# Optimization experiments

Hardware: AMD Instinct MI355X
Metric: run time of the kernel (lower is better)

The kernel has to match this reference:

```python
import jax, jax.numpy as jnp
import numpy as np

N_NODES = 20000
N_EDGES = 640000
NODE_DIM = 128
HIDDEN_DIM = 256
OUTPUT_DIM = 128


def setup_inputs() -> dict:
    key = jax.random.key(0)
    ks = jax.random.split(key, 10)
    x = jax.random.normal(ks[0], (N_NODES, NODE_DIM), dtype=jnp.float32)
    edge_index = jax.random.randint(ks[1], (2, N_EDGES), 0, N_NODES, dtype=jnp.int64)
    s1 = 1.0 / np.sqrt(2 * NODE_DIM)
    s1b = 1.0 / np.sqrt(HIDDEN_DIM)
    s2 = 1.0 / np.sqrt(2 * HIDDEN_DIM)
    s2b = 1.0 / np.sqrt(OUTPUT_DIM)
    # layer 1 MLP: Linear(2*node_dim, hidden) -> ReLU -> Linear(hidden, hidden)
    W1a = jax.random.uniform(ks[2], (2 * NODE_DIM, HIDDEN_DIM), jnp.float32, -s1, s1)
    b1a = jax.random.uniform(ks[3], (HIDDEN_DIM,), jnp.float32, -s1, s1)
    W1b = jax.random.uniform(ks[4], (HIDDEN_DIM, HIDDEN_DIM), jnp.float32, -s1b, s1b)
    b1b = jax.random.uniform(ks[5], (HIDDEN_DIM,), jnp.float32, -s1b, s1b)
    # layer 2 MLP: Linear(2*hidden, output) -> ReLU -> Linear(output, output)
    W2a = jax.random.uniform(ks[6], (2 * HIDDEN_DIM, OUTPUT_DIM), jnp.float32, -s2, s2)
    b2a = jax.random.uniform(ks[7], (OUTPUT_DIM,), jnp.float32, -s2, s2)
    W2b = jax.random.uniform(ks[8], (OUTPUT_DIM, OUTPUT_DIM), jnp.float32, -s2b, s2b)
    b2b = jax.random.uniform(ks[9], (OUTPUT_DIM,), jnp.float32, -s2b, s2b)
    return {"x": x, "edge_index": edge_index,
            "W1a": W1a, "b1a": b1a, "W1b": W1b, "b1b": b1b,
            "W2a": W2a, "b2a": b2a, "W2b": W2b, "b2b": b2b}


def _gnn_layer(x, src, dst, Wa, ba, Wb, bb):
    # PyG source_to_target: x_j = x[src], x_i = x[dst]; message on cat([x_i, x_j])
    h = jnp.concatenate([x[dst], x[src]], axis=-1)          # [E, 2D]
    m = jax.nn.relu(h @ Wa + ba) @ Wb + bb                  # [E, Dout]
    agg = jax.ops.segment_sum(m, dst, num_segments=N_NODES)  # [N, Dout]
    cnt = jax.ops.segment_sum(jnp.ones((m.shape[0],), m.dtype), dst,
                              num_segments=N_NODES)
    return agg / jnp.maximum(cnt, 1.0)[:, None]             # scatter-mean (0 if no edges)


def reference(x, edge_index, W1a, b1a, W1b, b1b, W2a, b2a, W2b, b2b):
    src = edge_index[0]
    dst = edge_index[1]
    h = jax.nn.relu(_gnn_layer(x, src, dst, W1a, b1a, W1b, b1b))
    out = _gnn_layer(h, src, dst, W2a, b2a, W2b, b2b)
    return out
```

## Files before the change

### kernel.cpp

```cpp
#include <hip/hip_runtime.h>


#define NODE_DIM 128
#define HID 256
#define OUTD 128
#define CPAD 16
#define SLOTS 128

typedef __attribute__((ext_vector_type(8))) _Float16 f16x8;
typedef __attribute__((ext_vector_type(4))) float f32x4;
typedef __attribute__((ext_vector_type(2))) _Float16 h2;

__device__ __forceinline__ h2 bc2(unsigned u) {
    return __builtin_bit_cast(h2, u);
}
__device__ __forceinline__ ushort f2h(float x) {
    _Float16 h = (_Float16)x;
    return __builtin_bit_cast(ushort, h);
}

__global__ void prep_all(const float* __restrict__ W1a, const float* __restrict__ W1b,
                         const float* __restrict__ W2a, const float* __restrict__ W2b,
                         ushort* __restrict__ T1a, ushort* __restrict__ T1b,
                         ushort* __restrict__ T2a, ushort* __restrict__ T2b,
                         int* __restrict__ cnt_p, int N) {
    int j = blockIdx.x * blockDim.x + threadIdx.x;
    if (j < 65536) {
        int n = j >> 7, k = j & 127;
        float v = (n < 256) ? W1a[k * 256 + n] : W1a[(128 + k) * 256 + (n - 256)];
        T1a[j] = f2h(v);
        return;
    }
    if (j < 131072) {
        int t = j - 65536;
        int n = t >> 8, k = t & 255;
        T1b[t] = f2h(W1b[k * 256 + n]);
        return;
    }
    if (j < 196608) {
        int t = j - 131072;
        int n = t >> 8, k = t & 255;
        float v = (n < 128) ? W2a[k * 128 + n] : W2a[(256 + k) * 128 + (n - 128)];
        T2a[t] = f2h(v);
        return;
    }
    if (j < 212992) {
        int t = j - 196608;
        int n = t >> 7, k = t & 127;
        T2b[t] = f2h(W2b[k * 128 + n]);
        return;
    }
    int k = j - 212992;
    if (k < N * CPAD) cnt_p[k] = 0;
}

__global__ void scatter_hist(const int* __restrict__ src, const int* __restrict__ dst,
                             int* __restrict__ cnt_p, int* __restrict__ csr, int E) {
    int e = (blockIdx.x * blockDim.x + threadIdx.x) * 2;
    if (e + 1 < E) {
        int2 s = *(const int2*)(src + e);
        int2 d = *(const int2*)(dst + e);
        int p0 = atomicAdd(&cnt_p[(size_t)d.x * CPAD], 1);
        if (p0 < SLOTS) csr[(size_t)d.x * SLOTS + p0] = s.x;
        int p1 = atomicAdd(&cnt_p[(size_t)d.y * CPAD], 1);
        if (p1 < SLOTS) csr[(size_t)d.y * SLOTS + p1] = s.y;
    } else if (e < E) {
        int p = atomicAdd(&cnt_p[(size_t)dst[e] * CPAD], 1);
        if (p < SLOTS) csr[(size_t)dst[e] * SLOTS + p] = src[e];
    }
}


#define GBM 128
#define GBN 128
#define GBK 32
#define LDSW 40

template <int MODE, int AF32>
__global__ __launch_bounds__(256) void gemm_h(
    const void* __restrict__ Av, int M, int K,
    const ushort* __restrict__ BT,
    const float* __restrict__ bias, const int* __restrict__ gate, int gstride,
    int relu, float* __restrict__ Cf, ushort* __restrict__ Ch, int Nc, int nsplit) {
    __shared__ ushort sA[GBM * LDSW];
    __shared__ ushort sB[GBN * LDSW];

    const int tid = threadIdx.x;
    const int lane = tid & 63;
    const int w = tid >> 6;
    const int wm = w >> 1, wn = w & 1;
    const int r16 = lane & 15, kg = lane >> 4;
    const int m0 = blockIdx.x * GBM;
    const int n0 = blockIdx.y * GBN;

    const int arow = tid >> 1, ahalf = tid & 1;

    f32x4 acc[4][4];
#pragma unroll
    for (int i = 0; i < 4; i++)
#pragma unroll
        for (int j = 0; j < 4; j++) acc[i][j] = (f32x4)0.f;

    for (int kt = 0; kt < K; kt += GBK) {
        {
            const int gr = m0 + arow;
            ushort* d = sA + arow * LDSW + ahalf * 16;
            if constexpr (AF32) {
                const float* Af = (const float*)Av;
                float4 v0 = make_float4(0.f, 0.f, 0.f, 0.f), v1 = v0, v2 = v0, v3 = v0;
                if (gr < M) {
                    const float* p = Af + (size_t)gr * K + kt + ahalf * 16;
                    v0 = ((const float4*)p)[0];
                    v1 = ((const float4*)p)[1];
                    v2 = ((const float4*)p)[2];
                    v3 = ((const float4*)p)[3];
                }
                ushort4 h0, h1, h2_, h3;
                h0.x = f2h(v0.x); h0.y = f2h(v0.y); h0.z = f2h(v0.z); h0.w = f2h(v0.w);
                h1.x = f2h(v1.x); h1.y = f2h(v1.y); h1.z = f2h(v1.z); h1.w = f2h(v1.w);
                h2_.x = f2h(v2.x); h2_.y = f2h(v2.y); h2_.z = f2h(v2.z); h2_.w = f2h(v2.w);
                h3.x = f2h(v3.x); h3.y = f2h(v3.y); h3.z = f2h(v3.z); h3.w = f2h(v3.w);
                ((ushort4*)d)[0] = h0;
                ((ushort4*)d)[1] = h1;
                ((ushort4*)d)[2] = h2_;
                ((ushort4*)d)[3] = h3;
            } else {
                const ushort* Ah = (const ushort*)Av;
                const size_t go = (size_t)gr * K + kt + ahalf * 16;
                int4 a0 = make_int4(0, 0, 0, 0), a1 = a0;
                if (gr < M) {
                    a0 = *(const int4*)(Ah + go);
                    a1 = *(const int4*)(Ah + go + 8);
                }
                *(int4*)(d) = a0;
                *(int4*)(d + 8) = a1;
            }
        }
        {
            const size_t go = (size_t)(n0 + arow) * K + kt + ahalf * 16;
            int4 b0 = *(const int4*)(BT + go);
            int4 b1 = *(const int4*)(BT + go + 8);
            ushort* d = sB + arow * LDSW + ahalf * 16;
            *(int4*)(d) = b0;
            *(int4*)(d + 8) = b1;
        }
        __syncthreads();

        f16x8 av[4], bv[4];
#pragma unroll
        for (int mi = 0; mi < 4; mi++)
            av[mi] = *(const f16x8*)(sA + (wm * 64 + mi * 16 + r16) * LDSW + kg * 8);
#pragma unroll
        for (int ni = 0; ni < 4; ni++)
            bv[ni] = *(const f16x8*)(sB + (wn * 64 + ni * 16 + r16) * LDSW + kg * 8);
#pragma unroll
        for (int mi = 0; mi < 4; mi++)
#pragma unroll
            for (int ni = 0; ni < 4; ni++)
                acc[mi][ni] = __builtin_amdgcn_mfma_f32_16x16x32_f16(av[mi], bv[ni], acc[mi][ni], 0, 0, 0);
        __syncthreads();
    }

#pragma unroll
    for (int ni = 0; ni < 4; ni++) {
        const int col = n0 + wn * 64 + ni * 16 + r16;
        float bv = 0.f;
        if constexpr (MODE == 1) {
            bv = (col < nsplit && bias) ? bias[col] : 0.f;
        } else {
            bv = bias ? bias[col] : 0.f;
        }
#pragma unroll
        for (int mi = 0; mi < 4; mi++) {
#pragma unroll
            for (int r = 0; r < 4; r++) {
                const int row = m0 + wm * 64 + mi * 16 + kg * 4 + r;
                if (row >= M) continue;
                if constexpr (MODE == 1) {
                    const float v = acc[mi][ni][r];
                    if (col < nsplit) {
                        Cf[(size_t)row * nsplit + col] = v + bv;
                    } else {
                        Ch[(size_t)row * (Nc - nsplit) + (col - nsplit)] = f2h(v);
                    }
                } else {
                    float g = 1.f;
                    if (gate) g = (gate[(size_t)row * gstride] > 0) ? 1.f : 0.f;
                    float v = acc[mi][ni][r] + bv * g;
                    if (relu) v = fmaxf(v, 0.f);
                    const size_t o = (size_t)row * Nc + col;
                    if constexpr (MODE == 0) {
                        Cf[o] = v;
                    } else {
                        Ch[o] = f2h(v);
                    }
                }
            }
        }
    }
}


template <int H>
__global__ __launch_bounds__(256) void agg_f(const float* __restrict__ Ptop,
                                             const ushort* __restrict__ Pbot,
                                             const int* __restrict__ cnt_p,
                                             const int* __restrict__ csr,
                                             ushort* __restrict__ S, int N) {
    constexpr int VPL = H / 64;
    __shared__ float red[2][64 * VPL];

    const int tid = threadIdx.x;
    const int lane = tid & 63;
    const int wv = __builtin_amdgcn_readfirstlane(tid >> 6);
    const int nb = wv >> 1;
    const int sub = wv & 1;
    int n = blockIdx.x * 2 + nb;
    if (n >= N) n = N - 1;

    int deg = cnt_p[(size_t)n * CPAD];
    if (deg > SLOTS) deg = SLOTS;
    const int begin = n * SLOTS;

    h2 t01, t23;
    if constexpr (VPL == 4) {
        float4 tf = *(const float4*)(Ptop + (size_t)n * H + lane * 4);
        t01 = (h2){(_Float16)tf.x, (_Float16)tf.y};
        t23 = (h2){(_Float16)tf.z, (_Float16)tf.w};
    } else {
        float2 tf = *(const float2*)(Ptop + (size_t)n * H + lane * 2);
        t01 = (h2){(_Float16)tf.x, (_Float16)tf.y};
        t23 = t01;
    }
    const h2 z2 = (h2)(_Float16)0.f;

    float a0 = 0.f, a1 = 0.f, a2 = 0.f, a3 = 0.f;
    const ushort* pb = Pbot + lane * VPL;

    const int Gf = deg >> 3;
    const int r = deg & 7;

    for (int g = sub; g < Gf; g += 2) {
        const int e = begin + g * 8;
        h2 p01 = z2, p23 = z2;
#pragma unroll
        for (int j = 0; j < 8; j++) {
            const int idx = csr[e + j];
            if constexpr (VPL == 4) {
                uint2 u = *(const uint2*)(pb + (size_t)idx * H);
                p01 += __builtin_elementwise_max(t01 + bc2(u.x), z2);
                p23 += __builtin_elementwise_max(t23 + bc2(u.y), z2);
            } else {
                unsigned u = *(const unsigned*)(pb + (size_t)idx * H);
                p01 += __builtin_elementwise_max(t01 + bc2(u), z2);
            }
        }
        a0 += (float)p01.x;
        a1 += (float)p01.y;
        if constexpr (VPL == 4) {
            a2 += (float)p23.x;
            a3 += (float)p23.y;
        }
    }
    if (r && sub == (Gf & 1)) {
        const int e = begin + Gf * 8;
        h2 p01 = z2, p23 = z2;
        for (int j = 0; j < r; j++) {
            const int idx = csr[e + j];
            if constexpr (VPL == 4) {
                uint2 u = *(const uint2*)(pb + (size_t)idx * H);
                p01 += __builtin_elementwise_max(t01 + bc2(u.x), z2);
                p23 += __builtin_elementwise_max(t23 + bc2(u.y), z2);
            } else {
                unsigned u = *(const unsigned*)(pb + (size_t)idx * H);
                p01 += __builtin_elementwise_max(t01 + bc2(u), z2);
            }
        }
        a0 += (float)p01.x;
        a1 += (float)p01.y;
        if constexpr (VPL == 4) {
            a2 += (float)p23.x;
            a3 += (float)p23.y;
        }
    }

    if (sub == 1) {
        red[nb][lane * VPL + 0] = a0;
        red[nb][lane * VPL + 1] = a1;
        if constexpr (VPL == 4) {
            red[nb][lane * VPL + 2] = a2;
            red[nb][lane * VPL + 3] = a3;
        }
    }
    __syncthreads();
    if (sub == 0) {
        a0 += red[nb][lane * VPL + 0];
        a1 += red[nb][lane * VPL + 1];
        if constexpr (VPL == 4) {
            a2 += red[nb][lane * VPL + 2];
            a3 += red[nb][lane * VPL + 3];
        }
        const float inv = (deg > 0) ? 1.f / (float)deg : 0.f;
        if constexpr (VPL == 4) {
            ushort4 h;
            h.x = f2h(a0 * inv);
            h.y = f2h(a1 * inv);
            h.z = f2h(a2 * inv);
            h.w = f2h(a3 * inv);
            *(ushort4*)(S + (size_t)n * H + lane * 4) = h;
        } else {
            ushort2 h;
            h.x = f2h(a0 * inv);
            h.y = f2h(a1 * inv);
            *(ushort2*)(S + (size_t)n * H + lane * 2) = h;
        }
    }
}


extern "C" void kernel_launch(void* const* d_in, const int* in_sizes, int n_in,
                              void* d_out, int out_size, void* d_ws, size_t ws_size,
                              hipStream_t stream) {
    const int N = in_sizes[0] / NODE_DIM;
    const int E = in_sizes[1] / 2;

    const float* x = (const float*)d_in[0];
    const int* ei = (const int*)d_in[1];
    const int* e_src = ei;
    const int* e_dst = ei + E;
    const float* W1a = (const float*)d_in[2];
    const float* b1a = (const float*)d_in[3];
    const float* W1b = (const float*)d_in[4];
    const float* b1b = (const float*)d_in[5];
    const float* W2a = (const float*)d_in[6];
    const float* b2a = (const float*)d_in[7];
    const float* W2b = (const float*)d_in[8];
    const float* b2b = (const float*)d_in[9];

    char* ws = (char*)d_ws;
    size_t off = 0;
    auto alloc = [&](size_t bytes) {
        size_t o = off;
        off += (bytes + 255) & ~(size_t)255;
        return o;
    };
    int* cnt_p = (int*)(ws + alloc((size_t)N * CPAD * 4));
    int* csr = (int*)(ws + alloc((size_t)N * SLOTS * 4));
    ushort* T1a = (ushort*)(ws + alloc((size_t)(2 * HID) * NODE_DIM * 2));
    ushort* T1b = (ushort*)(ws + alloc((size_t)HID * HID * 2));
    ushort* T2a = (ushort*)(ws + alloc((size_t)(2 * OUTD) * HID * 2));
    ushort* T2b = (ushort*)(ws + alloc((size_t)OUTD * OUTD * 2));
    float* P1t = (float*)(ws + alloc((size_t)N * HID * 4));
    ushort* P1b = (ushort*)(ws + alloc((size_t)N * HID * 2));
    ushort* P2b = (ushort*)(ws + alloc((size_t)N * OUTD * 2));
    ushort* S1 = (ushort*)(ws + alloc((size_t)N * HID * 2));
    ushort* S2 = (ushort*)(ws + alloc((size_t)N * OUTD * 2));
    ushort* h_h = (ushort*)(ws + alloc((size_t)N * HID * 2));
    float* P2t = P1t;

    const int MT = (N + GBM - 1) / GBM;
    const int AG = (N + 1) / 2;

    const int prep_n = 212992 + N * CPAD;
    prep_all<<<(prep_n + 255) / 256, 256, 0, stream>>>(
        W1a, W1b, W2a, W2b, T1a, T1b, T2a, T2b, cnt_p, N);

    scatter_hist<<<((E + 1) / 2 + 255) / 256, 256, 0, stream>>>(e_src, e_dst, cnt_p, csr, E);

    gemm_h<1, 1><<<dim3(MT, (2 * HID) / GBN), 256, 0, stream>>>(
        x, N, NODE_DIM, T1a, b1a, nullptr, 0, 0, P1t, P1b, 2 * HID, HID);

    agg_f<HID><<<AG, 256, 0, stream>>>(P1t, P1b, cnt_p, csr, S1, N);

    gemm_h<3, 0><<<dim3(MT, HID / GBN), 256, 0, stream>>>(
        S1, N, HID, T1b, b1b, cnt_p, CPAD, 1, nullptr, h_h, HID, 0);

    gemm_h<1, 0><<<dim3(MT, (2 * OUTD) / GBN), 256, 0, stream>>>(
        h_h, N, HID, T2a, b2a, nullptr, 0, 0, P2t, P2b, 2 * OUTD, OUTD);

    agg_f<OUTD><<<AG, 256, 0, stream>>>(P2t, P2b, cnt_p, csr, S2, N);

    gemm_h<0, 0><<<dim3(MT, OUTD / GBN), 256, 0, stream>>>(
        S2, N, OUTD, T2b, b2b, cnt_p, CPAD, 0, (float*)d_out, nullptr, OUTD, 0);
}
```

Before: 182.6 us.

## Slice aggregation by feature quarter per XCD with sentinel-padded neighbor lists

The aggregation kernel is rewritten so that each wave handles one node over a 64-feature slice. Blocks are mapped so that each XCD always works on the same feature slice, which keeps the gathered rows of that slice hot in its local L2. Neighbor lists are padded to multiples of 32 with a sentinel node index that points at an extra row filled with -inf half values, so the padded terms contribute zero after ReLU. This removes the remainder loop and the cross-wave LDS reduction and batches eight gathers before use. In exchange it adds a full csr initialization pass in the prep kernel, does up to 31 wasted gathers per node, and relies on blockIdx-to-XCD round-robin placement.

```diff
diff --git a/kernel.cpp b/kernel.cpp
--- a/kernel.cpp
+++ b/kernel.cpp
@@ -23,7 +23,9 @@
                          const float* __restrict__ W2a, const float* __restrict__ W2b,
                          ushort* __restrict__ T1a, ushort* __restrict__ T1b,
                          ushort* __restrict__ T2a, ushort* __restrict__ T2b,
-                         int* __restrict__ cnt_p, int N) {
+                         int* __restrict__ cnt_p, int N,
+                         ushort* __restrict__ P1b, ushort* __restrict__ P2b,
+                         int* __restrict__ csr) {
     int j = blockIdx.x * blockDim.x + threadIdx.x;
     if (j < 65536) {
         int n = j >> 7, k = j & 127;
@@ -51,7 +53,24 @@
         return;
     }
     int k = j - 212992;
-    if (k < N * CPAD) cnt_p[k] = 0;
+    if (k < N * CPAD) {
+        cnt_p[k] = 0;
+        return;
+    }
+    k -= N * CPAD;
+    if (k < HID) {
+        P1b[(size_t)N * HID + k] = 0xFC00;
+        return;
+    }
+    k -= HID;
+    if (k < OUTD) {
+        P2b[(size_t)N * OUTD + k] = 0xFC00;
+        return;
+    }
+    k -= OUTD;
+    if (k < N * SLOTS / 4) {
+        ((int4*)csr)[k] = make_int4(N, N, N, N);
+    }
 }
 
 __global__ void scatter_hist(const int* __restrict__ src, const int* __restrict__ dst,
@@ -202,118 +221,79 @@
 
 
 template <int H>
-__global__ __launch_bounds__(256) void agg_f(const float* __restrict__ Ptop,
+__global__ __launch_bounds__(256) void agg_s(const float* __restrict__ Ptop,
                                              const ushort* __restrict__ Pbot,
                                              const int* __restrict__ cnt_p,
                                              const int* __restrict__ csr,
                                              ushort* __restrict__ S, int N) {
-    constexpr int VPL = H / 64;
-    __shared__ float red[2][64 * VPL];
-
-    const int tid = threadIdx.x;
-    const int lane = tid & 63;
-    const int wv = __builtin_amdgcn_readfirstlane(tid >> 6);
-    const int nb = wv >> 1;
-    const int sub = wv & 1;
-    int n = blockIdx.x * 2 + nb;
-    if (n >= N) n = N - 1;
+    constexpr int SLICES = H / 64;
+    constexpr int XPS = 8 / SLICES;
+
+    const int bid = blockIdx.x;
+    const int xcd = bid & 7;
+    const int grp = bid >> 3;
+    const int slice = xcd / XPS;
+    const int subx = xcd % XPS;
+    const int wave = threadIdx.x >> 6;
+    const int lane = threadIdx.x & 63;
+
+    const int n = (grp * XPS + subx) * 4 + wave;
+    if (n >= N) return;
+    const int qoff = slice * 64;
+
+    const int fq = lane & 15;
+    const int es = lane >> 4;
 
     int deg = cnt_p[(size_t)n * CPAD];
     if (deg > SLOTS) deg = SLOTS;
+    const int dpad = (deg + 31) & ~31;
     const int begin = n * SLOTS;
 
-    h2 t01, t23;
-    if constexpr (VPL == 4) {
-        float4 tf = *(const float4*)(Ptop + (size_t)n * H + lane * 4);
-        t01 = (h2){(_Float16)tf.x, (_Float16)tf.y};
-        t23 = (h2){(_Float16)tf.z, (_Float16)tf.w};
-    } else {
-        float2 tf = *(const float2*)(Ptop + (size_t)n * H + lane * 2);
-        t01 = (h2){(_Float16)tf.x, (_Float16)tf.y};
-        t23 = t01;
-    }
+    const float4 tf = *(const float4*)(Ptop + (size_t)n * H + qoff + fq * 4);
+    const h2 t01 = (h2){(_Float16)tf.x, (_Float16)tf.y};
+    const h2 t23 = (h2){(_Float16)tf.z, (_Float16)tf.w};
     const h2 z2 = (h2)(_Float16)0.f;
 
     float a0 = 0.f, a1 = 0.f, a2 = 0.f, a3 = 0.f;
-    const ushort* pb = Pbot + lane * VPL;
-
-    const int Gf = deg >> 3;
-    const int r = deg & 7;
-
-    for (int g = sub; g < Gf; g += 2) {
-        const int e = begin + g * 8;
+    const ushort* pb = Pbot + qoff + fq * 4;
+
+    for (int e = begin; e < begin + dpad; e += 32) {
+        int idx[8];
+#pragma unroll
+        for (int j = 0; j < 8; j++) idx[j] = csr[e + j * 4 + es];
+        uint2 v[8];
+#pragma unroll
+        for (int j = 0; j < 8; j++)
+            v[j] = *(const uint2*)(pb + (size_t)idx[j] * H);
         h2 p01 = z2, p23 = z2;
 #pragma unroll
         for (int j = 0; j < 8; j++) {
-            const int idx = csr[e + j];
-            if constexpr (VPL == 4) {
-                uint2 u = *(const uint2*)(pb + (size_t)idx * H);
-                p01 += __builtin_elementwise_max(t01 + bc2(u.x), z2);
-                p23 += __builtin_elementwise_max(t23 + bc2(u.y), z2);
-            } else {
-                unsigned u = *(const unsigned*)(pb + (size_t)idx * H);
-                p01 += __builtin_elementwise_max(t01 + bc2(u), z2);
-            }
+            p01 += __builtin_elementwise_max(t01 + bc2(v[j].x), z2);
+            p23 += __builtin_elementwise_max(t23 + bc2(v[j].y), z2);
         }
         a0 += (float)p01.x;
         a1 += (float)p01.y;
-        if constexpr (VPL == 4) {
-            a2 += (float)p23.x;
-            a3 += (float)p23.y;
-        }
-    }
-    if (r && sub == (Gf & 1)) {
-        const int e = begin + Gf * 8;
-        h2 p01 = z2, p23 = z2;
-        for (int j = 0; j < r; j++) {
-            const int idx = csr[e + j];
-            if constexpr (VPL == 4) {
-                uint2 u = *(const uint2*)(pb + (size_t)idx * H);
-                p01 += __builtin_elementwise_max(t01 + bc2(u.x), z2);
-                p23 += __builtin_elementwise_max(t23 + bc2(u.y), z2);
-            } else {
-                unsigned u = *(const unsigned*)(pb + (size_t)idx * H);
-                p01 += __builtin_elementwise_max(t01 + bc2(u), z2);
-            }
-        }
-        a0 += (float)p01.x;
-        a1 += (float)p01.y;
-        if constexpr (VPL == 4) {
-            a2 += (float)p23.x;
-            a3 += (float)p23.y;
-        }
-    }
-
-    if (sub == 1) {
-        red[nb][lane * VPL + 0] = a0;
-        red[nb][lane * VPL + 1] = a1;
-        if constexpr (VPL == 4) {
-            red[nb][lane * VPL + 2] = a2;
-            red[nb][lane * VPL + 3] = a3;
-        }
-    }
-    __syncthreads();
-    if (sub == 0) {
-        a0 += red[nb][lane * VPL + 0];
-        a1 += red[nb][lane * VPL + 1];
-        if constexpr (VPL == 4) {
-            a2 += red[nb][lane * VPL + 2];
-            a3 += red[nb][lane * VPL + 3];
-        }
+        a2 += (float)p23.x;
+        a3 += (float)p23.y;
+    }
+
+    a0 += __shfl_xor(a0, 16, 64);
+    a1 += __shfl_xor(a1, 16, 64);
+    a2 += __shfl_xor(a2, 16, 64);
+    a3 += __shfl_xor(a3, 16, 64);
+    a0 += __shfl_xor(a0, 32, 64);
+    a1 += __shfl_xor(a1, 32, 64);
+    a2 += __shfl_xor(a2, 32, 64);
+    a3 += __shfl_xor(a3, 32, 64);
+
+    if (es == 0) {
         const float inv = (deg > 0) ? 1.f / (float)deg : 0.f;
-        if constexpr (VPL == 4) {
-            ushort4 h;
-            h.x = f2h(a0 * inv);
-            h.y = f2h(a1 * inv);
-            h.z = f2h(a2 * inv);
-            h.w = f2h(a3 * inv);
-            *(ushort4*)(S + (size_t)n * H + lane * 4) = h;
-        } else {
-            ushort2 h;
-            h.x = f2h(a0 * inv);
-            h.y = f2h(a1 * inv);
-            *(ushort2*)(S + (size_t)n * H + lane * 2) = h;
-        }
+        ushort4 h;
+        h.x = f2h(a0 * inv);
+        h.y = f2h(a1 * inv);
+        h.z = f2h(a2 * inv);
+        h.w = f2h(a3 * inv);
+        *(ushort4*)(S + (size_t)n * H + qoff + fq * 4) = h;
     }
 }
 
@@ -351,26 +331,27 @@
     ushort* T2a = (ushort*)(ws + alloc((size_t)(2 * OUTD) * HID * 2));
     ushort* T2b = (ushort*)(ws + alloc((size_t)OUTD * OUTD * 2));
     float* P1t = (float*)(ws + alloc((size_t)N * HID * 4));
-    ushort* P1b = (ushort*)(ws + alloc((size_t)N * HID * 2));
-    ushort* P2b = (ushort*)(ws + alloc((size_t)N * OUTD * 2));
+    ushort* P1b = (ushort*)(ws + alloc((size_t)(N + 1) * HID * 2));
+    ushort* P2b = (ushort*)(ws + alloc((size_t)(N + 1) * OUTD * 2));
     ushort* S1 = (ushort*)(ws + alloc((size_t)N * HID * 2));
     ushort* S2 = (ushort*)(ws + alloc((size_t)N * OUTD * 2));
     ushort* h_h = (ushort*)(ws + alloc((size_t)N * HID * 2));
     float* P2t = P1t;
 
     const int MT = (N + GBM - 1) / GBM;
-    const int AG = (N + 1) / 2;
-
-    const int prep_n = 212992 + N * CPAD;
+    const int AG1 = 8 * ((N + 4 * 2 - 1) / (4 * 2));
+    const int AG2 = 8 * ((N + 4 * 4 - 1) / (4 * 4));
+
+    const int prep_n = 212992 + N * CPAD + HID + OUTD + N * SLOTS / 4;
     prep_all<<<(prep_n + 255) / 256, 256, 0, stream>>>(
-        W1a, W1b, W2a, W2b, T1a, T1b, T2a, T2b, cnt_p, N);
+        W1a, W1b, W2a, W2b, T1a, T1b, T2a, T2b, cnt_p, N, P1b, P2b, csr);
 
     scatter_hist<<<((E + 1) / 2 + 255) / 256, 256, 0, stream>>>(e_src, e_dst, cnt_p, csr, E);
 
     gemm_h<1, 1><<<dim3(MT, (2 * HID) / GBN), 256, 0, stream>>>(
         x, N, NODE_DIM, T1a, b1a, nullptr, 0, 0, P1t, P1b, 2 * HID, HID);
 
-    agg_f<HID><<<AG, 256, 0, stream>>>(P1t, P1b, cnt_p, csr, S1, N);
+    agg_s<HID><<<AG1, 256, 0, stream>>>(P1t, P1b, cnt_p, csr, S1, N);
 
     gemm_h<3, 0><<<dim3(MT, HID / GBN), 256, 0, stream>>>(
         S1, N, HID, T1b, b1b, cnt_p, CPAD, 1, nullptr, h_h, HID, 0);
@@ -378,7 +359,7 @@
     gemm_h<1, 0><<<dim3(MT, (2 * OUTD) / GBN), 256, 0, stream>>>(
         h_h, N, HID, T2a, b2a, nullptr, 0, 0, P2t, P2b, 2 * OUTD, OUTD);
 
-    agg_f<OUTD><<<AG, 256, 0, stream>>>(P2t, P2b, cnt_p, csr, S2, N);
+    agg_s<OUTD><<<AG2, 256, 0, stream>>>(P2t, P2b, cnt_p, csr, S2, N);
 
     gemm_h<0, 0><<<dim3(MT, OUTD / GBN), 256, 0, stream>>>(
         S2, N, OUTD, T2b, b2b, cnt_p, CPAD, 0, (float*)d_out, nullptr, OUTD, 0);
```

New measurement: 187.7 us. 1.03x slower.
